# Performance work log

Hardware: AMD Instinct MI355X
Metric: run time of the kernel (lower is better)

The kernel has to match this reference:

```python
import jax, jax.numpy as jnp
import numpy as np

N_NODES = 100000
N_EDGES = 1600000
NFEAT, NHID, NCLASS = 512, 128, 40


def setup_inputs() -> dict:
    key = jax.random.key(0)
    ks = jax.random.split(key, 8)
    x = jax.random.normal(ks[0], (N_NODES, NFEAT), dtype=jnp.float32)
    adj_row = jax.random.randint(ks[1], (N_EDGES,), 0, N_NODES, dtype=jnp.int64)
    adj_col = jax.random.randint(ks[2], (N_EDGES,), 0, N_NODES, dtype=jnp.int64)
    adj_val = jax.random.uniform(ks[3], (N_EDGES,), dtype=jnp.float32)
    W1 = jax.random.normal(ks[4], (NFEAT, NHID), dtype=jnp.float32) * (1.0 / np.sqrt(NHID))
    b1 = jax.random.normal(ks[5], (NHID,), dtype=jnp.float32) * 0.01
    W2 = jax.random.normal(ks[6], (NHID, NCLASS), dtype=jnp.float32) * (1.0 / np.sqrt(NCLASS))
    b2 = jax.random.normal(ks[7], (NCLASS,), dtype=jnp.float32) * 0.01
    return {"x": x, "adj_row": adj_row, "adj_col": adj_col, "adj_val": adj_val,
            "W1": W1, "b1": b1, "W2": W2, "b2": b2}


def _spmm(row, col, val, dense):
    # COO SpMM: out[r] = sum_e val[e] * dense[col[e]]  for edges with row[e]==r
    gathered = val[:, None] * dense[col]          # [E, F]
    return jax.ops.segment_sum(gathered, row, num_segments=N_NODES)


def reference(x, adj_row, adj_col, adj_val, W1, b1, W2, b2):
    # Layer 1: support = X @ W1; out = A @ support + b1; ReLU
    h = _spmm(adj_row, adj_col, adj_val, x @ W1) + b1
    h = jax.nn.relu(h)
    # dropout is identity in eval mode (training=False)
    # Layer 2
    logits = _spmm(adj_row, adj_col, adj_val, h @ W2) + b2
    return jax.nn.log_softmax(logits, axis=1)
```

## Files before the change

kernel.cpp:

```cpp
#include <hip/hip_runtime.h>
#include <hip/hip_bf16.h>
#include <math.h>

#define N_NODES 100000
#define N_EDGES 1600000
#define NFEAT 512
#define NHID 128
#define NCLASS 40
#define CAP 48
#define G1_ROWS 128
#define G1_BLOCKS ((N_NODES + G1_ROWS - 1) / G1_ROWS)
#define HKW 256
#define PITCH2 264

#define BIN_ROWS 256
#define NBINS ((N_NODES + BIN_ROWS - 1) / BIN_ROWS)
#define EPB 4096
#define P1_BLOCKS ((N_EDGES + EPB - 1) / EPB)

typedef __attribute__((ext_vector_type(8))) short short8;
typedef __attribute__((ext_vector_type(4))) float floatx4;

__device__ __forceinline__ short f2bf(float f) {
    union { float f; unsigned u; } v; v.f = f;
    unsigned r = v.u + 0x7FFFu + ((v.u >> 16) & 1u);
    return (short)(r >> 16);
}
__device__ __forceinline__ float bf2f(unsigned short u) {
    union { unsigned u; float f; } v; v.u = ((unsigned)u) << 16;
    return v.f;
}
__device__ __forceinline__ unsigned pk2bf(float a, float b) {
    __hip_bfloat162 t = __float22bfloat162_rn(make_float2(a, b));
    union { __hip_bfloat162 h; unsigned u; } v; v.h = t;
    return v.u;
}

__global__ void convert_W1_kernel(const float* __restrict__ W1, unsigned short* __restrict__ W1T) {
    int i = blockIdx.x * 256 + threadIdx.x;
    int k = i >> 7, n = i & 127;
    W1T[(size_t)n * NFEAT + k] = (unsigned short)f2bf(W1[i]);
}

__global__ __launch_bounds__(256)
void p1_hist_kernel(const int* __restrict__ adj_row, int* __restrict__ blockHistT) {
    __shared__ int hh[NBINS];
    int t = threadIdx.x;
    for (int i = t; i < NBINS; i += 256) hh[i] = 0;
    __syncthreads();
    int base = blockIdx.x * EPB;
    #pragma unroll
    for (int i = 0; i < EPB / 256; i++) {
        int e = base + i * 256 + t;
        if (e < N_EDGES) atomicAdd(&hh[adj_row[e] >> 8], 1);
    }
    __syncthreads();
    for (int i = t; i < NBINS; i += 256)
        blockHistT[(size_t)i * P1_BLOCKS + blockIdx.x] = hh[i];
}

__global__ __launch_bounds__(512)
void p1_rowscan_kernel(int* __restrict__ blockHistT, int* __restrict__ rowTotal) {
    __shared__ int s[512];
    int b = blockIdx.x, t = threadIdx.x;
    int v = (t < P1_BLOCKS) ? blockHistT[(size_t)b * P1_BLOCKS + t] : 0;
    s[t] = v;
    __syncthreads();
    for (int ofs = 1; ofs < 512; ofs <<= 1) {
        int w = (t >= ofs) ? s[t - ofs] : 0;
        __syncthreads();
        s[t] += w;
        __syncthreads();
    }
    if (t < P1_BLOCKS) blockHistT[(size_t)b * P1_BLOCKS + t] = s[t] - v;
    if (t == 511) rowTotal[b] = s[511];
}

__global__ __launch_bounds__(512)
void p1_binscan_kernel(const int* __restrict__ rowTotal, int* __restrict__ binBase) {
    __shared__ int s[512];
    int t = threadIdx.x;
    int v = (t < NBINS) ? rowTotal[t] : 0;
    s[t] = v;
    __syncthreads();
    for (int ofs = 1; ofs < 512; ofs <<= 1) {
        int w = (t >= ofs) ? s[t - ofs] : 0;
        __syncthreads();
        s[t] += w;
        __syncthreads();
    }
    if (t < NBINS) binBase[t] = s[t] - v;
    if (t == 511) binBase[NBINS] = s[511];
}

__global__ __launch_bounds__(256)
void p1_scatter_kernel(const int* __restrict__ adj_row, const int* __restrict__ adj_col,
                       const float* __restrict__ adj_val,
                       const int* __restrict__ blockHistT, const int* __restrict__ binBase,
                       int2* __restrict__ recs) {
    __shared__ int cur[NBINS];
    int t = threadIdx.x;
    for (int i = t; i < NBINS; i += 256)
        cur[i] = blockHistT[(size_t)i * P1_BLOCKS + blockIdx.x] + binBase[i];
    __syncthreads();
    int base = blockIdx.x * EPB;
    #pragma unroll
    for (int i = 0; i < EPB / 256; i++) {
        int e = base + i * 256 + t;
        if (e < N_EDGES) {
            int r = adj_row[e];
            int pos = atomicAdd(&cur[r >> 8], 1);
            recs[pos] = make_int2(((r & 255) << 17) | adj_col[e],
                                  __float_as_int(adj_val[e]));
        }
    }
}

__global__ __launch_bounds__(256)
void p2_fill_kernel(const int2* __restrict__ recs, const int* __restrict__ binBase,
                    int* __restrict__ counts, int2* __restrict__ csr) {
    __shared__ int cnt[BIN_ROWS];
    int b = blockIdx.x, t = threadIdx.x;
    cnt[t] = 0;
    __syncthreads();
    int beg = binBase[b];
    int end = binBase[b + 1];
    for (int i = beg + t; i < end; i += 256) {
        int2 rec = recs[i];
        int rl = ((unsigned)rec.x) >> 17;
        int col = rec.x & 0x1FFFF;
        int rank = atomicAdd(&cnt[rl], 1);
        if (rank < CAP)
            csr[(size_t)(b * BIN_ROWS + rl) * CAP + rank] = make_int2(col, rec.y);
    }
    __syncthreads();
    int row = b * BIN_ROWS + t;
    if (row < N_NODES) counts[row] = cnt[t];
}

__global__ __launch_bounds__(512)
void gemm1_kernel(const float* __restrict__ x, const unsigned short* __restrict__ W1T,
                  unsigned short* __restrict__ out) {
    __shared__ unsigned short Bs[NHID * PITCH2];
    int t = threadIdx.x;
    int w = t >> 6, l = t & 63;
    int lane16 = l & 15, quad = l >> 4;
    int rowBase = blockIdx.x * G1_ROWS + w * 16;

    floatx4 acc[8];
    #pragma unroll
    for (int j = 0; j < 8; j++) acc[j] = (floatx4){0.f, 0.f, 0.f, 0.f};

    int gr = rowBase + lane16;
    if (gr >= N_NODES) gr = N_NODES - 1;

    for (int kh = 0; kh < 2; kh++) {
        if (kh) __syncthreads();
        {
            const unsigned short* src = W1T + kh * HKW;
            #pragma unroll
            for (int i = 0; i < 8; i++) {
                int c = t + i * 512;
                int n = c >> 5;
                int off = (c & 31) * 8;
                *(short8*)&Bs[n * PITCH2 + off] = *(const short8*)&src[(size_t)n * NFEAT + off];
            }
        }
        __syncthreads();
        const float* aRowH = x + (size_t)gr * NFEAT + kh * HKW + quad * 8;
        #pragma unroll 4
        for (int kc = 0; kc < HKW; kc += 32) {
            float4 v0 = *(const float4*)(aRowH + kc);
            float4 v1 = *(const float4*)(aRowH + kc + 4);
            union { short8 s; unsigned u[4]; } av;
            av.u[0] = pk2bf(v0.x, v0.y);
            av.u[1] = pk2bf(v0.z, v0.w);
            av.u[2] = pk2bf(v1.x, v1.y);
            av.u[3] = pk2bf(v1.z, v1.w);
            short8 afr = av.s;
            #pragma unroll
            for (int nt = 0; nt < 8; nt++) {
                short8 bfr = *(const short8*)&Bs[(nt * 16 + lane16) * PITCH2 + kc + quad * 8];
                acc[nt] = __builtin_amdgcn_mfma_f32_16x16x32_bf16(afr, bfr, acc[nt], 0, 0, 0);
            }
        }
    }
    #pragma unroll
    for (int r = 0; r < 4; r++) {
        int gr2 = rowBase + quad * 4 + r;
        if (gr2 < N_NODES) {
            #pragma unroll
            for (int nt = 0; nt < 8; nt++)
                out[(size_t)gr2 * NHID + nt * 16 + lane16] =
                    (unsigned short)f2bf(acc[nt][r]);
        }
    }
}

__global__ __launch_bounds__(256)
void spmmg_kernel(const int* __restrict__ counts, const int2* __restrict__ csr,
                  const unsigned short* __restrict__ dense, const float* __restrict__ b1,
                  const float* __restrict__ W2, unsigned short* __restrict__ out) {
    __shared__ float W2s[NHID * NCLASS];
    __shared__ unsigned hs32[32][64];
    int t = threadIdx.x;
    for (int i = t; i < NHID * NCLASS; i += 256) W2s[i] = W2[i];
    __syncthreads();
    int w = t >> 6, l = t & 63;
    int row0 = blockIdx.x * 32;
    float b1l0 = b1[l * 2 + 0], b1l1 = b1[l * 2 + 1];

    for (int k = 0; k < 8; k++) {
        int rs = __builtin_amdgcn_readfirstlane(row0 + w * 8 + k);
        int cnt = min(counts[rs], CAP);
        const int2* rowCsr = csr + (size_t)rs * CAP;
        float a0 = 0.f, a1 = 0.f;
        int j = 0;
        for (; j + 16 <= cnt; j += 16) {
            unsigned d[16];
            float v[16];
            #pragma unroll
            for (int q = 0; q < 16; q++) {
                int2 e = rowCsr[j + q];
                v[q] = __int_as_float(e.y);
                d[q] = *(const unsigned*)&dense[(size_t)e.x * NHID + l * 2];
            }
            #pragma unroll
            for (int q = 0; q < 16; q++) {
                a0 += v[q] * bf2f((unsigned short)d[q]);
                a1 += v[q] * bf2f((unsigned short)(d[q] >> 16));
            }
        }
        for (; j + 8 <= cnt; j += 8) {
            unsigned d[8];
            float v[8];
            #pragma unroll
            for (int q = 0; q < 8; q++) {
                int2 e = rowCsr[j + q];
                v[q] = __int_as_float(e.y);
                d[q] = *(const unsigned*)&dense[(size_t)e.x * NHID + l * 2];
            }
            #pragma unroll
            for (int q = 0; q < 8; q++) {
                a0 += v[q] * bf2f((unsigned short)d[q]);
                a1 += v[q] * bf2f((unsigned short)(d[q] >> 16));
            }
        }
        for (; j < cnt; j++) {
            int2 e = rowCsr[j];
            float v = __int_as_float(e.y);
            unsigned d = *(const unsigned*)&dense[(size_t)e.x * NHID + l * 2];
            a0 += v * bf2f((unsigned short)d);
            a1 += v * bf2f((unsigned short)(d >> 16));
        }
        hs32[w * 8 + k][l] = pk2bf(fmaxf(a0 + b1l0, 0.f), fmaxf(a1 + b1l1, 0.f));
    }
    if (l < NCLASS) {
        float acc[8];
        #pragma unroll
        for (int j = 0; j < 8; j++) acc[j] = 0.f;
        #pragma unroll 4
        for (int k2 = 0; k2 < NHID; k2 += 2) {
            float wk0 = W2s[k2 * NCLASS + l];
            float wk1 = W2s[(k2 + 1) * NCLASS + l];
            #pragma unroll
            for (int j = 0; j < 8; j++) {
                unsigned u = hs32[w * 8 + j][k2 >> 1];
                acc[j] += bf2f((unsigned short)u) * wk0
                        + bf2f((unsigned short)(u >> 16)) * wk1;
            }
        }
        #pragma unroll
        for (int j = 0; j < 8; j++)
            out[(size_t)(row0 + w * 8 + j) * NCLASS + l] = (unsigned short)f2bf(acc[j]);
    }
}

__global__ __launch_bounds__(256)
void spmm2_kernel(const int* __restrict__ counts, const int2* __restrict__ csr,
                  const unsigned short* __restrict__ dense, const float* __restrict__ b2,
                  float* __restrict__ out) {
    int rs = __builtin_amdgcn_readfirstlane(blockIdx.x * 4 + (threadIdx.x >> 6));
    int l = threadIdx.x & 63;
    int cnt = min(counts[rs], CAP);
    const int2* rowCsr = csr + (size_t)rs * CAP;
    float acc = 0.f;
    int j = 0;
    for (; j + 16 <= cnt; j += 16) {
        float v[16], f[16];
        #pragma unroll
        for (int q = 0; q < 16; q++) {
            int2 e = rowCsr[j + q];
            v[q] = __int_as_float(e.y);
            f[q] = (l < NCLASS) ? bf2f(dense[(size_t)e.x * NCLASS + l]) : 0.f;
        }
        #pragma unroll
        for (int q = 0; q < 16; q++) acc += v[q] * f[q];
    }
    for (; j + 8 <= cnt; j += 8) {
        float v[8], f[8];
        #pragma unroll
        for (int q = 0; q < 8; q++) {
            int2 e = rowCsr[j + q];
            v[q] = __int_as_float(e.y);
            f[q] = (l < NCLASS) ? bf2f(dense[(size_t)e.x * NCLASS + l]) : 0.f;
        }
        #pragma unroll
        for (int q = 0; q < 8; q++) acc += v[q] * f[q];
    }
    for (; j < cnt; j++) {
        int2 e = rowCsr[j];
        float v = __int_as_float(e.y);
        if (l < NCLASS) acc += v * bf2f(dense[(size_t)e.x * NCLASS + l]);
    }
    float logit = (l < NCLASS) ? (acc + b2[l]) : -INFINITY;
    float m = logit;
    #pragma unroll
    for (int o = 32; o >= 1; o >>= 1) m = fmaxf(m, __shfl_xor(m, o, 64));
    float e = (l < NCLASS) ? __expf(logit - m) : 0.f;
    float s = e;
    #pragma unroll
    for (int o = 32; o >= 1; o >>= 1) s += __shfl_xor(s, o, 64);
    if (l < NCLASS) out[(size_t)rs * NCLASS + l] = logit - m - __logf(s);
}


extern "C" void kernel_launch(void* const* d_in, const int* in_sizes, int n_in,
                              void* d_out, int out_size, void* d_ws, size_t ws_size,
                              hipStream_t stream) {
    const float* x       = (const float*)d_in[0];
    const int*   adj_row = (const int*)d_in[1];
    const int*   adj_col = (const int*)d_in[2];
    const float* adj_val = (const float*)d_in[3];
    const float* W1      = (const float*)d_in[4];
    const float* b1      = (const float*)d_in[5];
    const float* W2      = (const float*)d_in[6];
    const float* b2      = (const float*)d_in[7];
    float* out = (float*)d_out;

    char* ws = (char*)d_ws;
    size_t off = 0;
    auto alloc = [&](size_t bytes) -> void* {
        void* p = ws + off;
        off += bytes;
        off = (off + 255) & ~(size_t)255;
        return p;
    };
    unsigned short* support1 = (unsigned short*)alloc((size_t)N_NODES * NHID * 2);
    unsigned short* support2 = (unsigned short*)alloc((size_t)N_NODES * NCLASS * 2);
    unsigned short* W1T      = (unsigned short*)alloc((size_t)NFEAT * NHID * 2);
    int*   counts     = (int*)alloc((size_t)N_NODES * 4);
    int2*  csr        = (int2*)alloc((size_t)N_NODES * CAP * 8);
    int*   blockHistT = (int*)alloc((size_t)NBINS * P1_BLOCKS * 4);
    int*   rowTotal   = (int*)alloc((size_t)NBINS * 4);
    int*   binBase    = (int*)alloc((size_t)(NBINS + 1) * 4);
    int2*  recs       = (int2*)support1;

    convert_W1_kernel<<<(NFEAT * NHID) / 256, 256, 0, stream>>>(W1, W1T);
    p1_hist_kernel<<<P1_BLOCKS, 256, 0, stream>>>(adj_row, blockHistT);
    p1_rowscan_kernel<<<NBINS, 512, 0, stream>>>(blockHistT, rowTotal);
    p1_binscan_kernel<<<1, 512, 0, stream>>>(rowTotal, binBase);
    p1_scatter_kernel<<<P1_BLOCKS, 256, 0, stream>>>(adj_row, adj_col, adj_val,
                                                     blockHistT, binBase, recs);
    p2_fill_kernel<<<NBINS, 256, 0, stream>>>(recs, binBase, counts, csr);
    gemm1_kernel<<<G1_BLOCKS, 512, 0, stream>>>(x, W1T, support1);
    spmmg_kernel<<<N_NODES / 32, 256, 0, stream>>>(counts, csr, support1, b1, W2, support2);
    spmm2_kernel<<<N_NODES / 4, 256, 0, stream>>>(counts, csr, support2, b2, out);
}
```

Before: 591.7 us.

## Merge preprocessing launches by co-scheduling independent kernels and inlining bin scan

Fuses the W1 conversion into the histogram launch and the per-bin row scan into the GEMM1 launch by giving each role its own range of block indices. The single-block bin scan is removed; the scatter and fill kernels now each recompute the bin-base prefix scan redundantly in every block. recs gets its own workspace buffer instead of aliasing support1, so scatter can run after gemm1 without clobbering it. This cuts the launch count from nine to six and lets independent work overlap, at the cost of redundant scans and extra workspace memory.

```diff
diff --git a/kernel.cpp b/kernel.cpp
--- a/kernel.cpp
+++ b/kernel.cpp
@@ -17,6 +17,7 @@
 #define NBINS ((N_NODES + BIN_ROWS - 1) / BIN_ROWS)
 #define EPB 4096
 #define P1_BLOCKS ((N_EDGES + EPB - 1) / EPB)
+#define CONV_BLOCKS ((NFEAT * NHID) / 256)
 
 typedef __attribute__((ext_vector_type(8))) short short8;
 typedef __attribute__((ext_vector_type(4))) float floatx4;
@@ -36,116 +37,55 @@
     return v.u;
 }
 
-__global__ void convert_W1_kernel(const float* __restrict__ W1, unsigned short* __restrict__ W1T) {
-    int i = blockIdx.x * 256 + threadIdx.x;
-    int k = i >> 7, n = i & 127;
-    W1T[(size_t)n * NFEAT + k] = (unsigned short)f2bf(W1[i]);
-}
-
 __global__ __launch_bounds__(256)
-void p1_hist_kernel(const int* __restrict__ adj_row, int* __restrict__ blockHistT) {
-    __shared__ int hh[NBINS];
+void k1_hist_convert(const int* __restrict__ adj_row, int* __restrict__ blockHistT,
+                     const float* __restrict__ W1, unsigned short* __restrict__ W1T) {
     int t = threadIdx.x;
-    for (int i = t; i < NBINS; i += 256) hh[i] = 0;
-    __syncthreads();
-    int base = blockIdx.x * EPB;
-    #pragma unroll
-    for (int i = 0; i < EPB / 256; i++) {
-        int e = base + i * 256 + t;
-        if (e < N_EDGES) atomicAdd(&hh[adj_row[e] >> 8], 1);
-    }
-    __syncthreads();
-    for (int i = t; i < NBINS; i += 256)
-        blockHistT[(size_t)i * P1_BLOCKS + blockIdx.x] = hh[i];
+    if (blockIdx.x < P1_BLOCKS) {
+        __shared__ int hh[NBINS];
+        for (int i = t; i < NBINS; i += 256) hh[i] = 0;
+        __syncthreads();
+        int base = blockIdx.x * EPB;
+        #pragma unroll
+        for (int i = 0; i < EPB / 256; i++) {
+            int e = base + i * 256 + t;
+            if (e < N_EDGES) atomicAdd(&hh[adj_row[e] >> 8], 1);
+        }
+        __syncthreads();
+        for (int i = t; i < NBINS; i += 256)
+            blockHistT[(size_t)i * P1_BLOCKS + blockIdx.x] = hh[i];
+    } else {
+        int i = (blockIdx.x - P1_BLOCKS) * 256 + t;
+        int k = i >> 7, n = i & 127;
+        W1T[(size_t)n * NFEAT + k] = (unsigned short)f2bf(W1[i]);
+    }
 }
 
 __global__ __launch_bounds__(512)
-void p1_rowscan_kernel(int* __restrict__ blockHistT, int* __restrict__ rowTotal) {
-    __shared__ int s[512];
-    int b = blockIdx.x, t = threadIdx.x;
-    int v = (t < P1_BLOCKS) ? blockHistT[(size_t)b * P1_BLOCKS + t] : 0;
-    s[t] = v;
-    __syncthreads();
-    for (int ofs = 1; ofs < 512; ofs <<= 1) {
-        int w = (t >= ofs) ? s[t - ofs] : 0;
-        __syncthreads();
-        s[t] += w;
-        __syncthreads();
-    }
-    if (t < P1_BLOCKS) blockHistT[(size_t)b * P1_BLOCKS + t] = s[t] - v;
-    if (t == 511) rowTotal[b] = s[511];
-}
-
-__global__ __launch_bounds__(512)
-void p1_binscan_kernel(const int* __restrict__ rowTotal, int* __restrict__ binBase) {
-    __shared__ int s[512];
+void k2_gemm1_rowscan(const float* __restrict__ x, const unsigned short* __restrict__ W1T,
+                      unsigned short* __restrict__ out,
+                      int* __restrict__ blockHistT, int* __restrict__ rowTotal) {
+    __shared__ __align__(16) unsigned short Bs[NHID * PITCH2];
     int t = threadIdx.x;
-    int v = (t < NBINS) ? rowTotal[t] : 0;
-    s[t] = v;
-    __syncthreads();
-    for (int ofs = 1; ofs < 512; ofs <<= 1) {
-        int w = (t >= ofs) ? s[t - ofs] : 0;
-        __syncthreads();
-        s[t] += w;
-        __syncthreads();
-    }
-    if (t < NBINS) binBase[t] = s[t] - v;
-    if (t == 511) binBase[NBINS] = s[511];
-}
-
-__global__ __launch_bounds__(256)
-void p1_scatter_kernel(const int* __restrict__ adj_row, const int* __restrict__ adj_col,
-                       const float* __restrict__ adj_val,
-                       const int* __restrict__ blockHistT, const int* __restrict__ binBase,
-                       int2* __restrict__ recs) {
-    __shared__ int cur[NBINS];
-    int t = threadIdx.x;
-    for (int i = t; i < NBINS; i += 256)
-        cur[i] = blockHistT[(size_t)i * P1_BLOCKS + blockIdx.x] + binBase[i];
-    __syncthreads();
-    int base = blockIdx.x * EPB;
-    #pragma unroll
-    for (int i = 0; i < EPB / 256; i++) {
-        int e = base + i * 256 + t;
-        if (e < N_EDGES) {
-            int r = adj_row[e];
-            int pos = atomicAdd(&cur[r >> 8], 1);
-            recs[pos] = make_int2(((r & 255) << 17) | adj_col[e],
-                                  __float_as_int(adj_val[e]));
-        }
-    }
-}
-
-__global__ __launch_bounds__(256)
-void p2_fill_kernel(const int2* __restrict__ recs, const int* __restrict__ binBase,
-                    int* __restrict__ counts, int2* __restrict__ csr) {
-    __shared__ int cnt[BIN_ROWS];
-    int b = blockIdx.x, t = threadIdx.x;
-    cnt[t] = 0;
-    __syncthreads();
-    int beg = binBase[b];
-    int end = binBase[b + 1];
-    for (int i = beg + t; i < end; i += 256) {
-        int2 rec = recs[i];
-        int rl = ((unsigned)rec.x) >> 17;
-        int col = rec.x & 0x1FFFF;
-        int rank = atomicAdd(&cnt[rl], 1);
-        if (rank < CAP)
-            csr[(size_t)(b * BIN_ROWS + rl) * CAP + rank] = make_int2(col, rec.y);
-    }
-    __syncthreads();
-    int row = b * BIN_ROWS + t;
-    if (row < N_NODES) counts[row] = cnt[t];
-}
-
-__global__ __launch_bounds__(512)
-void gemm1_kernel(const float* __restrict__ x, const unsigned short* __restrict__ W1T,
-                  unsigned short* __restrict__ out) {
-    __shared__ unsigned short Bs[NHID * PITCH2];
-    int t = threadIdx.x;
+    if (blockIdx.x < NBINS) {
+        int* s = (int*)Bs;
+        int b = blockIdx.x;
+        int v = (t < P1_BLOCKS) ? blockHistT[(size_t)b * P1_BLOCKS + t] : 0;
+        s[t] = v;
+        __syncthreads();
+        for (int ofs = 1; ofs < 512; ofs <<= 1) {
+            int w = (t >= ofs) ? s[t - ofs] : 0;
+            __syncthreads();
+            s[t] += w;
+            __syncthreads();
+        }
+        if (t < P1_BLOCKS) blockHistT[(size_t)b * P1_BLOCKS + t] = s[t] - v;
+        if (t == 511) rowTotal[b] = s[511];
+        return;
+    }
     int w = t >> 6, l = t & 63;
     int lane16 = l & 15, quad = l >> 4;
-    int rowBase = blockIdx.x * G1_ROWS + w * 16;
+    int rowBase = (blockIdx.x - NBINS) * G1_ROWS + w * 16;
 
     floatx4 acc[8];
     #pragma unroll
@@ -195,6 +135,73 @@
                     (unsigned short)f2bf(acc[nt][r]);
         }
     }
+}
+
+__global__ __launch_bounds__(512)
+void p1_scatter_kernel(const int* __restrict__ adj_row, const int* __restrict__ adj_col,
+                       const float* __restrict__ adj_val,
+                       const int* __restrict__ blockHistT, const int* __restrict__ rowTotal,
+                       int2* __restrict__ recs) {
+    __shared__ int s[512];
+    __shared__ int binB[NBINS];
+    __shared__ int cur[NBINS];
+    int t = threadIdx.x;
+    int v = (t < NBINS) ? rowTotal[t] : 0;
+    s[t] = v;
+    __syncthreads();
+    for (int ofs = 1; ofs < 512; ofs <<= 1) {
+        int w = (t >= ofs) ? s[t - ofs] : 0;
+        __syncthreads();
+        s[t] += w;
+        __syncthreads();
+    }
+    if (t < NBINS) binB[t] = s[t] - v;
+    __syncthreads();
+    for (int i = t; i < NBINS; i += 512)
+        cur[i] = blockHistT[(size_t)i * P1_BLOCKS + blockIdx.x] + binB[i];
+    __syncthreads();
+    int base = blockIdx.x * EPB;
+    #pragma unroll
+    for (int i = 0; i < EPB / 512; i++) {
+        int e = base + i * 512 + t;
+        if (e < N_EDGES) {
+            int r = adj_row[e];
+            int pos = atomicAdd(&cur[r >> 8], 1);
+            recs[pos] = make_int2(((r & 255) << 17) | adj_col[e],
+                                  __float_as_int(adj_val[e]));
+        }
+    }
+}
+
+__global__ __launch_bounds__(512)
+void p2_fill_kernel(const int2* __restrict__ recs, const int* __restrict__ rowTotal,
+                    int* __restrict__ counts, int2* __restrict__ csr) {
+    __shared__ int s[512];
+    __shared__ int cnt[BIN_ROWS];
+    int b = blockIdx.x, t = threadIdx.x;
+    int v = (t < NBINS) ? rowTotal[t] : 0;
+    s[t] = v;
+    if (t < BIN_ROWS) cnt[t] = 0;
+    __syncthreads();
+    for (int ofs = 1; ofs < 512; ofs <<= 1) {
+        int w = (t >= ofs) ? s[t - ofs] : 0;
+        __syncthreads();
+        s[t] += w;
+        __syncthreads();
+    }
+    int beg = s[b] - rowTotal[b];
+    int end = s[b];
+    for (int i = beg + t; i < end; i += 512) {
+        int2 rec = recs[i];
+        int rl = ((unsigned)rec.x) >> 17;
+        int col = rec.x & 0x1FFFF;
+        int rank = atomicAdd(&cnt[rl], 1);
+        if (rank < CAP)
+            csr[(size_t)(b * BIN_ROWS + rl) * CAP + rank] = make_int2(col, rec.y);
+    }
+    __syncthreads();
+    int row = b * BIN_ROWS + t;
+    if (t < BIN_ROWS && row < N_NODES) counts[row] = cnt[t];
 }
 
 __global__ __launch_bounds__(256)
@@ -353,17 +360,14 @@
     int2*  csr        = (int2*)alloc((size_t)N_NODES * CAP * 8);
     int*   blockHistT = (int*)alloc((size_t)NBINS * P1_BLOCKS * 4);
     int*   rowTotal   = (int*)alloc((size_t)NBINS * 4);
-    int*   binBase    = (int*)alloc((size_t)(NBINS + 1) * 4);
-    int2*  recs       = (int2*)support1;
-
-    convert_W1_kernel<<<(NFEAT * NHID) / 256, 256, 0, stream>>>(W1, W1T);
-    p1_hist_kernel<<<P1_BLOCKS, 256, 0, stream>>>(adj_row, blockHistT);
-    p1_rowscan_kernel<<<NBINS, 512, 0, stream>>>(blockHistT, rowTotal);
-    p1_binscan_kernel<<<1, 512, 0, stream>>>(rowTotal, binBase);
-    p1_scatter_kernel<<<P1_BLOCKS, 256, 0, stream>>>(adj_row, adj_col, adj_val,
-                                                     blockHistT, binBase, recs);
-    p2_fill_kernel<<<NBINS, 256, 0, stream>>>(recs, binBase, counts, csr);
-    gemm1_kernel<<<G1_BLOCKS, 512, 0, stream>>>(x, W1T, support1);
+    int2*  recs       = (int2*)alloc((size_t)N_EDGES * 8);
+
+    k1_hist_convert<<<P1_BLOCKS + CONV_BLOCKS, 256, 0, stream>>>(adj_row, blockHistT, W1, W1T);
+    k2_gemm1_rowscan<<<NBINS + G1_BLOCKS, 512, 0, stream>>>(x, W1T, support1,
+                                                            blockHistT, rowTotal);
+    p1_scatter_kernel<<<P1_BLOCKS, 512, 0, stream>>>(adj_row, adj_col, adj_val,
+                                                     blockHistT, rowTotal, recs);
+    p2_fill_kernel<<<NBINS, 512, 0, stream>>>(recs, rowTotal, counts, csr);
     spmmg_kernel<<<N_NODES / 32, 256, 0, stream>>>(counts, csr, support1, b1, W2, support2);
     spmm2_kernel<<<N_NODES / 4, 256, 0, stream>>>(counts, csr, support2, b2, out);
 }
```

Result: faster. 573.3 us (-3.1%).
